# Performance work log

Measured on AMD Instinct MI355X. Metric: run time of the kernel, lower is better.

Reference implementation:

```python
import jax, jax.numpy as jnp
import numpy as np

N, E = 30000, 480000          # nodes, edges (avg degree 16)
DIM, DQK, H = 128, 128, 8     # dim_in = dim_v = 128, dim_qk = 128, heads
FD = DQK // H                 # kernel feature dim per head
DVH = DIM // H                # value dim per head


def setup_inputs() -> dict:
    key = jax.random.key(0)
    ks = jax.random.split(key, 12)
    g = lambda k, shape: jax.random.normal(k, shape, jnp.float32)
    return {
        "x": g(ks[0], (N, DIM)),
        "vec": g(ks[1], (N, 3, DIM)) * 0.1,
        "edge_vec": g(ks[2], (E, 3)),
        "edge_weight": jax.random.uniform(ks[3], (N, 1), jnp.float32),
        "W_fc1": g(ks[4], (DIM, 2 * DQK + DIM)) / np.sqrt(DIM),
        "W_fcv": g(ks[5], (DIM, 3 * DIM)) / np.sqrt(DIM),
        "b_fcv": jnp.zeros((3 * DIM,), jnp.float32),
        "W_fco": g(ks[6], (DIM, DIM)) / np.sqrt(DIM),
        "b_fco": jnp.zeros((DIM,), jnp.float32),
        "W_out": g(ks[7], (DIM, 3 * DIM)) / np.sqrt(DIM),
        "W_vecproj": g(ks[8], (DIM, 3 * DIM)) / np.sqrt(DIM),
        "W_equiv": g(ks[9], (DIM, DIM)) / np.sqrt(DIM),
        "ln_scale": jnp.ones((DIM,), jnp.float32),
        "ln_bias": jnp.zeros((DIM,), jnp.float32),
        "edge_index": jax.random.randint(ks[10], (2, E), 0, N),
    }


def _phi(z):
    # positive kernel feature map (elu + 1), per head: [N, DQK] -> [N, H, FD]
    return jax.nn.elu(z.reshape(z.shape[0], H, FD)) + 1.0


def reference(x, vec, edge_vec, edge_weight,
              W_fc1, W_fcv, b_fcv, W_fco, b_fco, W_out, W_vecproj, W_equiv,
              ln_scale, ln_bias, edge_index):
    # fc_1 -> q | k | non-attention residual
    h1 = x @ W_fc1
    q, k, non_att = h1[:, :DQK], h1[:, DQK:2 * DQK], h1[:, 2 * DQK:]
    # fc_v -> v | vec1 gate | vec2 gate
    pv = x @ W_fcv + b_fcv
    v, vec1, vec2 = pv[:, :DIM], pv[:, DIM:2 * DIM], pv[:, 2 * DIM:]

    # kernelized linear self-attention over the node set (order 1->1)
    qf, kf = _phi(q), _phi(k)                      # [N,H,FD]
    vh = v.reshape(N, H, DVH)                      # [N,H,DVH]
    kv = jnp.einsum('nhf,nhd->hfd', kf, vh)        # [H,FD,DVH]
    z = kf.sum(0)                                  # [H,FD]
    num = jnp.einsum('nhf,hfd->nhd', qf, kv)
    den = jnp.einsum('nhf,hf->nh', qf, z)[..., None] + 1e-6
    att = (num / den).reshape(N, DIM)

    # equivariant vector projections: v1p, v2p, v3p
    vp = jnp.einsum('nci,io->nco', vec, W_vecproj)  # [N,3,3*DIM]
    v1p, v2p, v3p = vp[..., :DIM], vp[..., DIM:2 * DIM], vp[..., 2 * DIM:]
    vec_dot = (v1p * v2p).sum(1)                    # [N,DIM]

    # MPNN propagate: per-edge vector messages, scatter-sum to destination
    src, dst = edge_index[0], edge_index[1]
    msg = vec[src] * vec1[src][:, None, :] + edge_vec[:, :, None] * vec2[src][:, None, :]
    vec_agg = jax.ops.segment_sum(msg, dst, num_segments=N)  # [N,3,DIM]

    # gated output combination (o1, o2, o3)
    o = att @ W_out
    o1, o2, o3 = o[:, :DIM], o[:, DIM:2 * DIM], o[:, 2 * DIM:]
    delta_x = vec_dot * o2 + o3
    delta_vec = v3p * o1[:, None, :] + vec_agg

    att_out = ((att + delta_x) @ W_fco + b_fco) * edge_weight
    out_x = non_att + att_out

    # LayerNorm over channel dim, then equivariant projection
    mu = delta_vec.mean(-1, keepdims=True)
    var = delta_vec.var(-1, keepdims=True)
    dvn = (delta_vec - mu) / jnp.sqrt(var + 1e-5) * ln_scale + ln_bias
    out_vec = dvn @ W_equiv
    return out_x, out_vec
```

## Files before the change

### kernel.cpp

```cpp
#include <hip/hip_runtime.h>
#include <math.h>

#define NN 30000
#define EE 480000
#define DIM 128
#define KVB 512

typedef __attribute__((ext_vector_type(8))) short bf16x8;
typedef __attribute__((ext_vector_type(4))) short s16x4;
typedef __attribute__((ext_vector_type(4))) float f32x4;
typedef __attribute__((ext_vector_type(4))) float float4v;

__device__ inline short f2bf(float f) {
    union { float f; unsigned u; } v; v.f = f;
    unsigned u = v.u;
    u += 0x7fffu + ((u >> 16) & 1u);
    return (short)(u >> 16);
}
__device__ inline float bf2f(unsigned short u) {
    union { unsigned u; float f; } v; v.u = ((unsigned)u) << 16; return v.f;
}

__device__ inline bf16x8 cvt8(float4v lo, float4v hi) {
    bf16x8 r;
    r[0] = f2bf(lo[0]); r[1] = f2bf(lo[1]); r[2] = f2bf(lo[2]); r[3] = f2bf(lo[3]);
    r[4] = f2bf(hi[0]); r[5] = f2bf(hi[1]); r[6] = f2bf(hi[2]); r[7] = f2bf(hi[3]);
    return r;
}

__global__ void pack_all(const float* __restrict__ fc1, const float* __restrict__ fcv,
                         const float* __restrict__ wout, const float* __restrict__ wvp,
                         const float* __restrict__ fco, const float* __restrict__ weq,
                         short* __restrict__ Wpk) {
    int fid = blockIdx.x * 4 + (threadIdx.x >> 6);
    int lane = threadIdx.x & 63;
    const float* src; int Nsrc, c0, f;
    if (fid < 96)       { src = fc1;  Nsrc = 384; c0 = 0;   f = fid; }
    else if (fid < 192) { src = fcv;  Nsrc = 384; c0 = 0;   f = fid - 96; }
    else if (fid < 288) { src = wout; Nsrc = 384; c0 = 0;   f = fid - 192; }
    else if (fid < 352) { src = wvp;  Nsrc = 384; c0 = 0;   f = fid - 288; }
    else if (fid < 384) { src = wvp;  Nsrc = 384; c0 = 256; f = fid - 352; }
    else if (fid < 416) { src = fco;  Nsrc = 128; c0 = 0;   f = fid - 384; }
    else                { src = weq;  Nsrc = 128; c0 = 0;   f = fid - 416; }
    int ct = f >> 2, kk = f & 3;
    int k0 = kk * 32 + (lane >> 4) * 8;
    int col = c0 + ct * 16 + (lane & 15);
    bf16x8 v;
#pragma unroll
    for (int i = 0; i < 8; ++i) v[i] = f2bf(src[(size_t)(k0 + i) * Nsrc + col]);
    *(bf16x8*)(Wpk + ((size_t)fid * 64 + lane) * 8) = v;
}

template<int COLS, int CT_PER, bool BIAS, typename InT, typename OutT>
__global__ __launch_bounds__(256) void mfma_gemm(const InT* __restrict__ in,
        const short* __restrict__ Wpk, const float* __restrict__ bias,
        OutT* __restrict__ out, int nrows) {
    const int lane = threadIdx.x & 63;
    const int wid = threadIdx.x >> 6;
    const int rbase = blockIdx.x * 128 + wid * 32;
    if (rbase >= nrows) return;
    const int ct0 = blockIdx.y * CT_PER;
    const int rlo = lane & 15, khi = (lane >> 4) * 8;
    bf16x8 a[2][4];
#pragma unroll
    for (int t = 0; t < 2; ++t) {
        int row = min(rbase + t * 16 + rlo, nrows - 1);
        const InT* rp = in + (size_t)row * 128 + khi;
#pragma unroll
        for (int kk = 0; kk < 4; ++kk) {
            if constexpr (sizeof(InT) == 4) {
                float4v lo = *(const float4v*)(rp + kk * 32);
                float4v hi = *(const float4v*)(rp + kk * 32 + 4);
                a[t][kk] = cvt8(lo, hi);
            } else {
                a[t][kk] = *(const bf16x8*)(rp + kk * 32);
            }
        }
    }
#pragma unroll
    for (int c = 0; c < CT_PER; ++c) {
        const int ct = ct0 + c;
        bf16x8 b[4];
#pragma unroll
        for (int kk = 0; kk < 4; ++kk)
            b[kk] = *(const bf16x8*)(Wpk + ((size_t)(ct * 4 + kk) * 64 + lane) * 8);
        f32x4 acc0 = {0.f, 0.f, 0.f, 0.f}, acc1 = {0.f, 0.f, 0.f, 0.f};
#pragma unroll
        for (int kk = 0; kk < 4; ++kk) {
            acc0 = __builtin_amdgcn_mfma_f32_16x16x32_bf16(a[0][kk], b[kk], acc0, 0, 0, 0);
            acc1 = __builtin_amdgcn_mfma_f32_16x16x32_bf16(a[1][kk], b[kk], acc1, 0, 0, 0);
        }
        const int col = ct * 16 + rlo;
        const float bv = BIAS ? bias[col] : 0.f;
#pragma unroll
        for (int r = 0; r < 4; ++r) {
            int row0 = rbase + (lane >> 4) * 4 + r;
            int row1 = row0 + 16;
            if constexpr (sizeof(OutT) == 4) {
                if (row0 < nrows) out[(size_t)row0 * COLS + col] = acc0[r] + bv;
                if (row1 < nrows) out[(size_t)row1 * COLS + col] = acc1[r] + bv;
            } else {
                if (row0 < nrows) out[(size_t)row0 * COLS + col] = (OutT)f2bf(acc0[r] + bv);
                if (row1 < nrows) out[(size_t)row1 * COLS + col] = (OutT)f2bf(acc1[r] + bv);
            }
        }
    }
}

__global__ __launch_bounds__(256) void kv_part(const float* __restrict__ h1,
        const float* __restrict__ pv, float* __restrict__ slab) {
    __shared__ float kf_s[8][DIM];
    __shared__ float v_s[8][DIM];
    const int tid = threadIdx.x;
    const int rpb = (NN + KVB - 1) / KVB;
    const int n0 = blockIdx.x * rpb;
    const int n1 = min(n0 + rpb, NN);
    const int base = tid * 8;
    const int hf = base >> 4;
    const int h = hf >> 4;
    const int d0 = base & 15;
    const int lr = tid >> 5;
    const int lg = tid & 31;
    const bool isK = lg < 16;
    const int le = (lg & 15) * 8;
    float acc[8];
#pragma unroll
    for (int i = 0; i < 8; ++i) acc[i] = 0.f;
    float zacc = 0.f;
    float4v p0 = {0,0,0,0}, p1 = {0,0,0,0};
    bool pvalid = false;
    {
        int n = n0 + lr;
        pvalid = n < n1;
        if (pvalid) {
            const float* src = isK ? (h1 + (size_t)n * 384 + 128 + le)
                                   : (pv + (size_t)n * 384 + le);
            p0 = *(const float4v*)src;
            p1 = *(const float4v*)(src + 4);
        }
    }
    for (int nt = n0; nt < n1; nt += 8) {
        __syncthreads();
        float4v c0 = p0, c1 = p1;
        if (!pvalid) { c0 = {0,0,0,0}; c1 = {0,0,0,0}; }
        else if (isK) {
#pragma unroll
            for (int i = 0; i < 4; ++i) {
                c0[i] = c0[i] > 0.f ? c0[i] + 1.f : expf(c0[i]);
                c1[i] = c1[i] > 0.f ? c1[i] + 1.f : expf(c1[i]);
            }
        }
        float* dst = (isK ? kf_s[lr] : v_s[lr]) + le;
        *(float4v*)dst = c0;
        *(float4v*)(dst + 4) = c1;
        __syncthreads();
        {
            int n = nt + 8 + lr;
            pvalid = n < n1;
            if (pvalid) {
                const float* src = isK ? (h1 + (size_t)n * 384 + 128 + le)
                                       : (pv + (size_t)n * 384 + le);
                p0 = *(const float4v*)src;
                p1 = *(const float4v*)(src + 4);
            }
        }
#pragma unroll
        for (int r = 0; r < 8; ++r) {
            float kfv = kf_s[r][hf];
#pragma unroll
            for (int i = 0; i < 8; ++i) acc[i] = fmaf(kfv, v_s[r][h * 16 + d0 + i], acc[i]);
            if (tid < 128) zacc += kf_s[r][tid];
        }
    }
    float* row = slab + (size_t)blockIdx.x * 2176;
#pragma unroll
    for (int i = 0; i < 8; ++i) row[base + i] = acc[i];
    if (tid < 128) row[2048 + tid] = zacc;
}

__global__ void kv_final(const float* __restrict__ slab, float* __restrict__ kvz) {
    int i = blockIdx.x * 256 + threadIdx.x;
    if (i >= 2176) return;
    float a[8];
#pragma unroll
    for (int j = 0; j < 8; ++j) a[j] = 0.f;
    for (int b = 0; b < KVB; b += 8) {
#pragma unroll
        for (int j = 0; j < 8; ++j) a[j] += slab[(size_t)(b + j) * 2176 + i];
    }
    kvz[i] = ((a[0] + a[1]) + (a[2] + a[3])) + ((a[4] + a[5]) + (a[6] + a[7]));
}

__global__ void attn_apply(const float* __restrict__ h1, const float* __restrict__ kvz,
                           unsigned short* __restrict__ att) {
    __shared__ float kv_s[8 * 16 * 17];
    __shared__ float z_s[DIM];
    __shared__ float qf_s[8][DIM];
    const int tid = threadIdx.x;
    const int n0 = blockIdx.x * 8;
    for (int i = tid; i < 2048; i += 128) {
        int hf = i >> 4, d = i & 15;
        kv_s[hf * 17 + d] = kvz[i];
    }
    z_s[tid] = kvz[2048 + tid];
#pragma unroll
    for (int r = 0; r < 8; ++r) {
        float qv = h1[(size_t)(n0 + r) * 384 + tid];
        qf_s[r][tid] = qv > 0.f ? qv + 1.f : expf(qv);
    }
    __syncthreads();
    const int h = tid >> 4, d = tid & 15;
#pragma unroll
    for (int r = 0; r < 8; ++r) {
        float num = 0.f, den = 0.f;
#pragma unroll
        for (int f = 0; f < 16; ++f) {
            float q = qf_s[r][h * 16 + f];
            num = fmaf(q, kv_s[(h * 16 + f) * 17 + d], num);
            den = fmaf(q, z_s[h * 16 + f], den);
        }
        att[(size_t)(n0 + r) * DIM + tid] = (unsigned short)f2bf(num / (den + 1e-6f));
    }
}

__global__ void vecdot_reduce(const unsigned short* __restrict__ vp12,
                              const float* __restrict__ vec, const float* __restrict__ pv,
                              float* __restrict__ vdot, unsigned short* __restrict__ P) {
    const int tid = threadIdx.x;
    const int n0 = blockIdx.x * 8;
#pragma unroll
    for (int r = 0; r < 8; ++r) {
        int n = n0 + r;
        const unsigned short* vp = vp12 + (size_t)(3 * n) * 256;
        float acc = bf2f(vp[tid]) * bf2f(vp[128 + tid])
                  + bf2f(vp[256 + tid]) * bf2f(vp[384 + tid])
                  + bf2f(vp[512 + tid]) * bf2f(vp[640 + tid]);
        vdot[(size_t)n * DIM + tid] = acc;
        float v1 = pv[(size_t)n * 384 + 128 + tid];
        float v2 = pv[(size_t)n * 384 + 256 + tid];
        s16x4 pk;
        pk[0] = f2bf(v2);
        pk[1] = f2bf(vec[((size_t)n * 3 + 0) * DIM + tid] * v1);
        pk[2] = f2bf(vec[((size_t)n * 3 + 1) * DIM + tid] * v1);
        pk[3] = f2bf(vec[((size_t)n * 3 + 2) * DIM + tid] * v1);
        *(s16x4*)(P + (size_t)n * 512 + tid * 4) = pk;
    }
}

__global__ void hist_kernel(const int* __restrict__ eidx, int* __restrict__ cnt) {
    int e = blockIdx.x * 256 + threadIdx.x;
    if (e < EE) atomicAdd(&cnt[eidx[EE + e]], 1);
}

__global__ void scan_kernel(const int* __restrict__ cnt, int* __restrict__ off,
                            int* __restrict__ pos) {
    __shared__ int wsum[16];
    const int tid = threadIdx.x;
    const int lane = tid & 63, wv = tid >> 6;
    const int PER = 30;
    const int base = tid * PER;
    int local[PER];
    int s = 0;
#pragma unroll
    for (int i = 0; i < PER; ++i) {
        int idx = base + i;
        int c = (idx < NN) ? cnt[idx] : 0;
        local[i] = s;
        s += c;
    }
    int incl = s;
#pragma unroll
    for (int d = 1; d < 64; d <<= 1) {
        int v = __shfl_up(incl, d, 64);
        if (lane >= d) incl += v;
    }
    if (lane == 63) wsum[wv] = incl;
    __syncthreads();
    if (wv == 0 && lane < 16) {
        int v = wsum[lane];
        int iv = v;
#pragma unroll
        for (int d = 1; d < 16; d <<= 1) {
            int u = __shfl_up(iv, d, 16);
            if (lane >= d) iv += u;
        }
        wsum[lane] = iv - v;
    }
    __syncthreads();
    const int carry = wsum[wv] + (incl - s);
#pragma unroll
    for (int i = 0; i < PER; ++i) {
        int idx = base + i;
        if (idx < NN) {
            int v = carry + local[i];
            off[idx] = v;
            pos[idx] = v;
        }
    }
    if (tid == 1023) off[NN] = wsum[15] + incl;
}

__global__ void scatter_kernel(const int* __restrict__ eidx, const float* __restrict__ evec,
                               int* __restrict__ pos, int4* __restrict__ sorted4) {
    int e = blockIdx.x * 256 + threadIdx.x;
    if (e >= EE) return;
    int dst = eidx[EE + e];
    int src = eidx[e];
    float e0 = evec[(size_t)e * 3 + 0];
    float e1 = evec[(size_t)e * 3 + 1];
    float e2 = evec[(size_t)e * 3 + 2];
    int p = atomicAdd(&pos[dst], 1);
    sorted4[p] = make_int4(src, __float_as_int(e0), __float_as_int(e1), __float_as_int(e2));
}

__global__ __launch_bounds__(256) void edge_agg_kernel(
        const int* __restrict__ off, const int4* __restrict__ sorted4,
        const unsigned short* __restrict__ P, float* __restrict__ agg) {
    __shared__ int srcs[128];
    __shared__ float evs[3][128];
    __shared__ float part[3][128];
    const int dst = blockIdx.x;
    const int tid = threadIdx.x;
    const int g = tid >> 7, o = tid & 127;
    const int j0 = off[dst], j1 = off[dst + 1];
    float a0 = 0.f, a1 = 0.f, a2 = 0.f;
    for (int jt = j0; jt < j1; jt += 128) {
        const int m = min(128, j1 - jt);
        if (tid < m) {
            int4 w = sorted4[jt + tid];
            srcs[tid] = w.x;
            evs[0][tid] = __int_as_float(w.y);
            evs[1][tid] = __int_as_float(w.z);
            evs[2][tid] = __int_as_float(w.w);
        }
        __syncthreads();
        int jj = g;
        for (; jj + 14 < m; jj += 16) {
            s16x4 pk[8];
#pragma unroll
            for (int u = 0; u < 8; ++u)
                pk[u] = *(const s16x4*)(P + (size_t)srcs[jj + 2 * u] * 512 + o * 4);
#pragma unroll
            for (int u = 0; u < 8; ++u) {
                float v2 = bf2f((unsigned short)pk[u][0]);
                a0 += fmaf(evs[0][jj + 2 * u], v2, bf2f((unsigned short)pk[u][1]));
                a1 += fmaf(evs[1][jj + 2 * u], v2, bf2f((unsigned short)pk[u][2]));
                a2 += fmaf(evs[2][jj + 2 * u], v2, bf2f((unsigned short)pk[u][3]));
            }
        }
        for (; jj < m; jj += 2) {
            s16x4 pk = *(const s16x4*)(P + (size_t)srcs[jj] * 512 + o * 4);
            float v2 = bf2f((unsigned short)pk[0]);
            a0 += fmaf(evs[0][jj], v2, bf2f((unsigned short)pk[1]));
            a1 += fmaf(evs[1][jj], v2, bf2f((unsigned short)pk[2]));
            a2 += fmaf(evs[2][jj], v2, bf2f((unsigned short)pk[3]));
        }
        __syncthreads();
    }
    if (g == 1) { part[0][o] = a0; part[1][o] = a1; part[2][o] = a2; }
    __syncthreads();
    if (g == 0) {
        a0 += part[0][o]; a1 += part[1][o]; a2 += part[2][o];
        agg[((size_t)dst * 3 + 0) * DIM + o] = a0;
        agg[((size_t)dst * 3 + 1) * DIM + o] = a1;
        agg[((size_t)dst * 3 + 2) * DIM + o] = a2;
    }
}

__global__ __launch_bounds__(256) void outx_mfma(const unsigned short* __restrict__ att,
        const float* __restrict__ vdot, const float* __restrict__ o,
        const short* __restrict__ Wpk, const float* __restrict__ bfco,
        const float* __restrict__ h1, const float* __restrict__ ew,
        float* __restrict__ outx) {
    const int lane = threadIdx.x & 63;
    const int wid = threadIdx.x >> 6;
    const int rbase = blockIdx.x * 128 + wid * 32;
    if (rbase >= NN) return;
    const int ct0 = blockIdx.y * 4;
    const int rlo = lane & 15, khi = (lane >> 4) * 8;
    bf16x8 a[2][4];
#pragma unroll
    for (int t = 0; t < 2; ++t) {
        int row = min(rbase + t * 16 + rlo, NN - 1);
        const unsigned short* pa = att + (size_t)row * 128 + khi;
        const float* pd = vdot + (size_t)row * 128 + khi;
        const float* po = o + (size_t)row * 384 + khi;
#pragma unroll
        for (int kk = 0; kk < 4; ++kk) {
            int kb = kk * 32;
            bf16x8 av = *(const bf16x8*)(pa + kb);
            float4v al, ah;
#pragma unroll
            for (int i = 0; i < 4; ++i) {
                al[i] = bf2f((unsigned short)av[i]);
                ah[i] = bf2f((unsigned short)av[4 + i]);
            }
            float4v dl = *(const float4v*)(pd + kb), dh = *(const float4v*)(pd + kb + 4);
            float4v o2l = *(const float4v*)(po + kb + 128), o2h = *(const float4v*)(po + kb + 132);
            float4v o3l = *(const float4v*)(po + kb + 256), o3h = *(const float4v*)(po + kb + 260);
            a[t][kk] = cvt8(al + dl * o2l + o3l, ah + dh * o2h + o3h);
        }
    }
    float ewv[2][4];
#pragma unroll
    for (int t = 0; t < 2; ++t)
#pragma unroll
        for (int r = 0; r < 4; ++r)
            ewv[t][r] = ew[min(rbase + t * 16 + (lane >> 4) * 4 + r, NN - 1)];
#pragma unroll
    for (int c = 0; c < 4; ++c) {
        const int ct = ct0 + c;
        bf16x8 b[4];
#pragma unroll
        for (int kk = 0; kk < 4; ++kk)
            b[kk] = *(const bf16x8*)(Wpk + ((size_t)(ct * 4 + kk) * 64 + lane) * 8);
        f32x4 acc0 = {0.f, 0.f, 0.f, 0.f}, acc1 = {0.f, 0.f, 0.f, 0.f};
#pragma unroll
        for (int kk = 0; kk < 4; ++kk) {
            acc0 = __builtin_amdgcn_mfma_f32_16x16x32_bf16(a[0][kk], b[kk], acc0, 0, 0, 0);
            acc1 = __builtin_amdgcn_mfma_f32_16x16x32_bf16(a[1][kk], b[kk], acc1, 0, 0, 0);
        }
        const int col = ct * 16 + rlo;
        const float bv = bfco[col];
#pragma unroll
        for (int r = 0; r < 4; ++r) {
            int row0 = rbase + (lane >> 4) * 4 + r;
            if (row0 < NN)
                outx[(size_t)row0 * 128 + col] =
                    h1[(size_t)row0 * 384 + 256 + col] + (acc0[r] + bv) * ewv[0][r];
            int row1 = row0 + 16;
            if (row1 < NN)
                outx[(size_t)row1 * 128 + col] =
                    h1[(size_t)row1 * 384 + 256 + col] + (acc1[r] + bv) * ewv[1][r];
        }
    }
}

__global__ __launch_bounds__(256) void outvec1(const float* __restrict__ vec,
        const short* __restrict__ Wpk3, const float* __restrict__ o,
        const float* __restrict__ agg, const float* __restrict__ ln_scale,
        const float* __restrict__ ln_bias, unsigned short* __restrict__ dvn) {
    const int NR = 3 * NN;
    const int lane = threadIdx.x & 63;
    const int wid = threadIdx.x >> 6;
    const int rbase = blockIdx.x * 128 + wid * 32;
    if (rbase >= NR) return;
    const int rlo = lane & 15, khi = (lane >> 4) * 8;
    bf16x8 a[2][4];
#pragma unroll
    for (int t = 0; t < 2; ++t) {
        int row = min(rbase + t * 16 + rlo, NR - 1);
        const float* rp = vec + (size_t)row * 128 + khi;
#pragma unroll
        for (int kk = 0; kk < 4; ++kk) {
            float4v lo = *(const float4v*)(rp + kk * 32);
            float4v hi = *(const float4v*)(rp + kk * 32 + 4);
            a[t][kk] = cvt8(lo, hi);
        }
    }
    f32x4 acc[2][8];
#pragma unroll
    for (int ct = 0; ct < 8; ++ct) {
        bf16x8 b[4];
#pragma unroll
        for (int kk = 0; kk < 4; ++kk)
            b[kk] = *(const bf16x8*)(Wpk3 + ((size_t)(ct * 4 + kk) * 64 + lane) * 8);
        f32x4 a0 = {0.f, 0.f, 0.f, 0.f}, a1 = {0.f, 0.f, 0.f, 0.f};
#pragma unroll
        for (int kk = 0; kk < 4; ++kk) {
            a0 = __builtin_amdgcn_mfma_f32_16x16x32_bf16(a[0][kk], b[kk], a0, 0, 0, 0);
            a1 = __builtin_amdgcn_mfma_f32_16x16x32_bf16(a[1][kk], b[kk], a1, 0, 0, 0);
        }
        acc[0][ct] = a0; acc[1][ct] = a1;
    }
    float s[2][4], s2[2][4];
#pragma unroll
    for (int t = 0; t < 2; ++t)
#pragma unroll
        for (int r = 0; r < 4; ++r) { s[t][r] = 0.f; s2[t][r] = 0.f; }
#pragma unroll
    for (int t = 0; t < 2; ++t)
#pragma unroll
        for (int r = 0; r < 4; ++r) {
            int row = min(rbase + t * 16 + (lane >> 4) * 4 + r, NR - 1);
            int n = row / 3;
#pragma unroll
            for (int ct = 0; ct < 8; ++ct) {
                int col = ct * 16 + rlo;
                float dv = acc[t][ct][r] * o[(size_t)n * 384 + col]
                         + agg[(size_t)row * 128 + col];
                acc[t][ct][r] = dv;
                s[t][r] += dv;
                s2[t][r] = fmaf(dv, dv, s2[t][r]);
            }
        }
#pragma unroll
    for (int t = 0; t < 2; ++t)
#pragma unroll
        for (int r = 0; r < 4; ++r) {
#pragma unroll
            for (int m = 1; m < 16; m <<= 1) {
                s[t][r] += __shfl_xor(s[t][r], m, 16);
                s2[t][r] += __shfl_xor(s2[t][r], m, 16);
            }
        }
#pragma unroll
    for (int t = 0; t < 2; ++t)
#pragma unroll
        for (int r = 0; r < 4; ++r) {
            int row = rbase + t * 16 + (lane >> 4) * 4 + r;
            if (row >= NR) continue;
            float mu = s[t][r] * (1.f / 128.f);
            float rstd = rsqrtf(s2[t][r] * (1.f / 128.f) - mu * mu + 1e-5f);
#pragma unroll
            for (int ct = 0; ct < 8; ++ct) {
                int col = ct * 16 + rlo;
                dvn[(size_t)row * 128 + col] =
                    (unsigned short)f2bf(fmaf((acc[t][ct][r] - mu) * rstd, ln_scale[col], ln_bias[col]));
            }
        }
}

extern "C" void kernel_launch(void* const* d_in, const int* in_sizes, int n_in,
                              void* d_out, int out_size, void* d_ws, size_t ws_size,
                              hipStream_t stream) {
    const float* x          = (const float*)d_in[0];
    const float* vec        = (const float*)d_in[1];
    const float* edge_vec   = (const float*)d_in[2];
    const float* edge_weight= (const float*)d_in[3];
    const float* W_fc1      = (const float*)d_in[4];
    const float* W_fcv      = (const float*)d_in[5];
    const float* b_fcv      = (const float*)d_in[6];
    const float* W_fco      = (const float*)d_in[7];
    const float* b_fco      = (const float*)d_in[8];
    const float* W_out      = (const float*)d_in[9];
    const float* W_vecproj  = (const float*)d_in[10];
    const float* W_equiv    = (const float*)d_in[11];
    const float* ln_scale   = (const float*)d_in[12];
    const float* ln_bias    = (const float*)d_in[13];
    const int*   edge_index = (const int*)d_in[14];

    float* out_x   = (float*)d_out;
    float* out_vec = out_x + (size_t)NN * DIM;
    unsigned short* Pb = (unsigned short*)d_out;

    float* ws   = (float*)d_ws;
    float* h1   = ws;
    float* pv   = h1 + 11520000;
    float* att  = pv + 11520000;
    float* vdot = att + 3840000;
    float* o    = vdot + 3840000;
    float* agg  = o + 11520000;
    float* kvz  = agg + 11520000;
    unsigned short* att_b = (unsigned short*)att;
    unsigned short* vp12b = (unsigned short*)o;
    unsigned short* dvnb  = (unsigned short*)pv;
    float* slab = agg;
    int* cnt    = (int*)(kvz + 2176);
    int* off    = cnt + NN;
    int* pos    = off + NN + 1;
    size_t soff = ((size_t)(pos + NN - (int*)ws) + 3) & ~(size_t)3;
    int4* sorted4 = (int4*)((int*)ws + soff);
    short* Wpk  = (short*)((int*)ws + soff + (size_t)4 * EE);
    short* pk_fc1  = Wpk;
    short* pk_fcv  = Wpk + 96 * 512;
    short* pk_wout = Wpk + 192 * 512;
    short* pk_vp12 = Wpk + 288 * 512;
    short* pk_vp3  = Wpk + 352 * 512;
    short* pk_fco  = Wpk + 384 * 512;
    short* pk_weq  = Wpk + 416 * 512;

    hipMemsetAsync(cnt, 0, NN * sizeof(int), stream);

    pack_all<<<112, 256, 0, stream>>>(W_fc1, W_fcv, W_out, W_vecproj, W_fco, W_equiv, Wpk);

    hist_kernel<<<(EE + 255) / 256, 256, 0, stream>>>(edge_index, cnt);
    scan_kernel<<<1, 1024, 0, stream>>>(cnt, off, pos);
    scatter_kernel<<<(EE + 255) / 256, 256, 0, stream>>>(edge_index, edge_vec, pos, sorted4);

    const int gN = (NN + 127) / 128;
    const int g3N = (3 * NN + 127) / 128;
    mfma_gemm<384, 8, false, float, float><<<dim3(gN, 3), 256, 0, stream>>>(x, pk_fc1, nullptr, h1, NN);
    mfma_gemm<384, 8, true, float, float><<<dim3(gN, 3), 256, 0, stream>>>(x, pk_fcv, b_fcv, pv, NN);
    kv_part<<<KVB, 256, 0, stream>>>(h1, pv, slab);
    kv_final<<<9, 256, 0, stream>>>(slab, kvz);
    attn_apply<<<NN / 8, 128, 0, stream>>>(h1, kvz, att_b);
    mfma_gemm<256, 8, false, float, unsigned short><<<dim3(g3N, 2), 256, 0, stream>>>(vec, pk_vp12, nullptr, vp12b, 3 * NN);
    vecdot_reduce<<<NN / 8, 128, 0, stream>>>(vp12b, vec, pv, vdot, Pb);
    mfma_gemm<384, 8, false, unsigned short, float><<<dim3(gN, 3), 256, 0, stream>>>(att_b, pk_wout, nullptr, o, NN);
    edge_agg_kernel<<<NN, 256, 0, stream>>>(off, sorted4, Pb, agg);
    outx_mfma<<<dim3(gN, 2), 256, 0, stream>>>(att_b, vdot, o, pk_fco, b_fco, h1, edge_weight, out_x);
    outvec1<<<g3N, 256, 0, stream>>>(vec, pk_vp3, o, agg, ln_scale, ln_bias, dvnb);
    mfma_gemm<128, 4, false, unsigned short, float><<<dim3(g3N, 2), 256, 0, stream>>>(dvnb, pk_weq, nullptr, out_vec, 3 * NN);
}
```

Baseline: 454.0 us.

## Compute v3p once in merged vecproj GEMM and store intermediates in bf16

Merges the v1p/v2p and v3p projections into one GEMM that writes bf16 vp12 and v3p, so outvec no longer recomputes the v3p GEMM. The LayerNorm stage becomes a lightweight elementwise kernel. The o, vdot and agg intermediates are stored as bf16 instead of fp32 to cut memory traffic. edge_agg is split across two blocks per destination with four edge groups, and vecdot_reduce uses vectorised loads. This adds bf16 rounding to more intermediates, which costs some precision.

```diff
diff --git a/kernel.cpp b/kernel.cpp
--- a/kernel.cpp
+++ b/kernel.cpp
@@ -7,9 +7,11 @@
 #define KVB 512
 
 typedef __attribute__((ext_vector_type(8))) short bf16x8;
+typedef __attribute__((ext_vector_type(8))) short s16x8;
 typedef __attribute__((ext_vector_type(4))) short s16x4;
 typedef __attribute__((ext_vector_type(4))) float f32x4;
 typedef __attribute__((ext_vector_type(4))) float float4v;
+typedef unsigned short ushort_t;
 
 __device__ inline short f2bf(float f) {
     union { float f; unsigned u; } v; v.f = f;
@@ -20,12 +22,22 @@
 __device__ inline float bf2f(unsigned short u) {
     union { unsigned u; float f; } v; v.u = ((unsigned)u) << 16; return v.f;
 }
+__device__ inline unsigned pack2(float a, float b) {
+    return (unsigned)(ushort_t)f2bf(a) | ((unsigned)(ushort_t)f2bf(b) << 16);
+}
 
 __device__ inline bf16x8 cvt8(float4v lo, float4v hi) {
     bf16x8 r;
     r[0] = f2bf(lo[0]); r[1] = f2bf(lo[1]); r[2] = f2bf(lo[2]); r[3] = f2bf(lo[3]);
     r[4] = f2bf(hi[0]); r[5] = f2bf(hi[1]); r[6] = f2bf(hi[2]); r[7] = f2bf(hi[3]);
     return r;
+}
+__device__ inline void bf8_to_f(bf16x8 v, float4v& lo, float4v& hi) {
+#pragma unroll
+    for (int i = 0; i < 4; ++i) {
+        lo[i] = bf2f((unsigned short)v[i]);
+        hi[i] = bf2f((unsigned short)v[4 + i]);
+    }
 }
 
 __global__ void pack_all(const float* __restrict__ fc1, const float* __restrict__ fcv,
@@ -107,6 +119,56 @@
     }
 }
 
+__global__ __launch_bounds__(256) void vp_gemm(const float* __restrict__ in,
+        const short* __restrict__ Wpk, ushort_t* __restrict__ vp12,
+        ushort_t* __restrict__ v3p, int nrows) {
+    const int lane = threadIdx.x & 63;
+    const int wid = threadIdx.x >> 6;
+    const int rbase = blockIdx.x * 128 + wid * 32;
+    if (rbase >= nrows) return;
+    const int ct0 = blockIdx.y * 8;
+    const int rlo = lane & 15, khi = (lane >> 4) * 8;
+    bf16x8 a[2][4];
+#pragma unroll
+    for (int t = 0; t < 2; ++t) {
+        int row = min(rbase + t * 16 + rlo, nrows - 1);
+        const float* rp = in + (size_t)row * 128 + khi;
+#pragma unroll
+        for (int kk = 0; kk < 4; ++kk) {
+            float4v lo = *(const float4v*)(rp + kk * 32);
+            float4v hi = *(const float4v*)(rp + kk * 32 + 4);
+            a[t][kk] = cvt8(lo, hi);
+        }
+    }
+#pragma unroll
+    for (int c = 0; c < 8; ++c) {
+        const int ct = ct0 + c;
+        bf16x8 b[4];
+#pragma unroll
+        for (int kk = 0; kk < 4; ++kk)
+            b[kk] = *(const bf16x8*)(Wpk + ((size_t)(ct * 4 + kk) * 64 + lane) * 8);
+        f32x4 acc0 = {0.f, 0.f, 0.f, 0.f}, acc1 = {0.f, 0.f, 0.f, 0.f};
+#pragma unroll
+        for (int kk = 0; kk < 4; ++kk) {
+            acc0 = __builtin_amdgcn_mfma_f32_16x16x32_bf16(a[0][kk], b[kk], acc0, 0, 0, 0);
+            acc1 = __builtin_amdgcn_mfma_f32_16x16x32_bf16(a[1][kk], b[kk], acc1, 0, 0, 0);
+        }
+        const int col = ct * 16 + rlo;
+#pragma unroll
+        for (int r = 0; r < 4; ++r) {
+            int row0 = rbase + (lane >> 4) * 4 + r;
+            int row1 = row0 + 16;
+            if (col < 256) {
+                if (row0 < nrows) vp12[(size_t)row0 * 256 + col] = (ushort_t)f2bf(acc0[r]);
+                if (row1 < nrows) vp12[(size_t)row1 * 256 + col] = (ushort_t)f2bf(acc1[r]);
+            } else {
+                if (row0 < nrows) v3p[(size_t)row0 * 128 + col - 256] = (ushort_t)f2bf(acc0[r]);
+                if (row1 < nrows) v3p[(size_t)row1 * 128 + col - 256] = (ushort_t)f2bf(acc1[r]);
+            }
+        }
+    }
+}
+
 __global__ __launch_bounds__(256) void kv_part(const float* __restrict__ h1,
         const float* __restrict__ pv, float* __restrict__ slab) {
     __shared__ float kf_s[8][DIM];
@@ -192,7 +254,7 @@
 }
 
 __global__ void attn_apply(const float* __restrict__ h1, const float* __restrict__ kvz,
-                           unsigned short* __restrict__ att) {
+                           ushort_t* __restrict__ att) {
     __shared__ float kv_s[8 * 16 * 17];
     __shared__ float z_s[DIM];
     __shared__ float qf_s[8][DIM];
@@ -219,31 +281,41 @@
             num = fmaf(q, kv_s[(h * 16 + f) * 17 + d], num);
             den = fmaf(q, z_s[h * 16 + f], den);
         }
-        att[(size_t)(n0 + r) * DIM + tid] = (unsigned short)f2bf(num / (den + 1e-6f));
-    }
-}
-
-__global__ void vecdot_reduce(const unsigned short* __restrict__ vp12,
-                              const float* __restrict__ vec, const float* __restrict__ pv,
-                              float* __restrict__ vdot, unsigned short* __restrict__ P) {
+        att[(size_t)(n0 + r) * DIM + tid] = (ushort_t)f2bf(num / (den + 1e-6f));
+    }
+}
+
+__global__ __launch_bounds__(256) void vecdot_reduce(const ushort_t* __restrict__ vp12,
+        const float* __restrict__ vec, const float* __restrict__ pv,
+        ushort_t* __restrict__ vdot, ushort_t* __restrict__ P) {
     const int tid = threadIdx.x;
+    const int c2 = tid & 63;
+    const int sub = tid >> 6;
     const int n0 = blockIdx.x * 8;
 #pragma unroll
-    for (int r = 0; r < 8; ++r) {
-        int n = n0 + r;
-        const unsigned short* vp = vp12 + (size_t)(3 * n) * 256;
-        float acc = bf2f(vp[tid]) * bf2f(vp[128 + tid])
-                  + bf2f(vp[256 + tid]) * bf2f(vp[384 + tid])
-                  + bf2f(vp[512 + tid]) * bf2f(vp[640 + tid]);
-        vdot[(size_t)n * DIM + tid] = acc;
-        float v1 = pv[(size_t)n * 384 + 128 + tid];
-        float v2 = pv[(size_t)n * 384 + 256 + tid];
-        s16x4 pk;
-        pk[0] = f2bf(v2);
-        pk[1] = f2bf(vec[((size_t)n * 3 + 0) * DIM + tid] * v1);
-        pk[2] = f2bf(vec[((size_t)n * 3 + 1) * DIM + tid] * v1);
-        pk[3] = f2bf(vec[((size_t)n * 3 + 2) * DIM + tid] * v1);
-        *(s16x4*)(P + (size_t)n * 512 + tid * 4) = pk;
+    for (int rr = 0; rr < 2; ++rr) {
+        const int n = n0 + sub + rr * 4;
+        float a0 = 0.f, a1 = 0.f;
+#pragma unroll
+        for (int c = 0; c < 3; ++c) {
+            unsigned u1 = *(const unsigned*)(vp12 + (size_t)(3 * n + c) * 256 + 2 * c2);
+            unsigned u2 = *(const unsigned*)(vp12 + (size_t)(3 * n + c) * 256 + 128 + 2 * c2);
+            a0 = fmaf(bf2f((unsigned short)u1), bf2f((unsigned short)u2), a0);
+            a1 = fmaf(bf2f((unsigned short)(u1 >> 16)), bf2f((unsigned short)(u2 >> 16)), a1);
+        }
+        *(unsigned*)(vdot + (size_t)n * 128 + 2 * c2) = pack2(a0, a1);
+        float2 v1 = *(const float2*)(pv + (size_t)n * 384 + 128 + 2 * c2);
+        float2 v2 = *(const float2*)(pv + (size_t)n * 384 + 256 + 2 * c2);
+        s16x8 pk;
+        pk[0] = f2bf(v2.x);
+        pk[4] = f2bf(v2.y);
+#pragma unroll
+        for (int c = 0; c < 3; ++c) {
+            float2 vc = *(const float2*)(vec + ((size_t)n * 3 + c) * 128 + 2 * c2);
+            pk[1 + c] = f2bf(vc.x * v1.x);
+            pk[5 + c] = f2bf(vc.y * v1.y);
+        }
+        *(s16x8*)(P + (size_t)n * 512 + (size_t)c2 * 8) = pk;
     }
 }
 
@@ -315,13 +387,14 @@
 
 __global__ __launch_bounds__(256) void edge_agg_kernel(
         const int* __restrict__ off, const int4* __restrict__ sorted4,
-        const unsigned short* __restrict__ P, float* __restrict__ agg) {
+        const ushort_t* __restrict__ P, ushort_t* __restrict__ agg) {
     __shared__ int srcs[128];
     __shared__ float evs[3][128];
-    __shared__ float part[3][128];
+    __shared__ float part[3][3][64];
     const int dst = blockIdx.x;
     const int tid = threadIdx.x;
-    const int g = tid >> 7, o = tid & 127;
+    const int g = tid >> 6, l = tid & 63;
+    const int o = blockIdx.y * 64 + l;
     const int j0 = off[dst], j1 = off[dst + 1];
     float a0 = 0.f, a1 = 0.f, a2 = 0.f;
     for (int jt = j0; jt < j1; jt += 128) {
@@ -335,20 +408,21 @@
         }
         __syncthreads();
         int jj = g;
-        for (; jj + 14 < m; jj += 16) {
+        for (; jj + 28 < m; jj += 32) {
             s16x4 pk[8];
 #pragma unroll
             for (int u = 0; u < 8; ++u)
-                pk[u] = *(const s16x4*)(P + (size_t)srcs[jj + 2 * u] * 512 + o * 4);
+                pk[u] = *(const s16x4*)(P + (size_t)srcs[jj + 4 * u] * 512 + o * 4);
 #pragma unroll
             for (int u = 0; u < 8; ++u) {
+                int e = jj + 4 * u;
                 float v2 = bf2f((unsigned short)pk[u][0]);
-                a0 += fmaf(evs[0][jj + 2 * u], v2, bf2f((unsigned short)pk[u][1]));
-                a1 += fmaf(evs[1][jj + 2 * u], v2, bf2f((unsigned short)pk[u][2]));
-                a2 += fmaf(evs[2][jj + 2 * u], v2, bf2f((unsigned short)pk[u][3]));
+                a0 += fmaf(evs[0][e], v2, bf2f((unsigned short)pk[u][1]));
+                a1 += fmaf(evs[1][e], v2, bf2f((unsigned short)pk[u][2]));
+                a2 += fmaf(evs[2][e], v2, bf2f((unsigned short)pk[u][3]));
             }
         }
-        for (; jj < m; jj += 2) {
+        for (; jj < m; jj += 4) {
             s16x4 pk = *(const s16x4*)(P + (size_t)srcs[jj] * 512 + o * 4);
             float v2 = bf2f((unsigned short)pk[0]);
             a0 += fmaf(evs[0][jj], v2, bf2f((unsigned short)pk[1]));
@@ -357,18 +431,20 @@
         }
         __syncthreads();
     }
-    if (g == 1) { part[0][o] = a0; part[1][o] = a1; part[2][o] = a2; }
+    if (g) { part[g - 1][0][l] = a0; part[g - 1][1][l] = a1; part[g - 1][2][l] = a2; }
     __syncthreads();
     if (g == 0) {
-        a0 += part[0][o]; a1 += part[1][o]; a2 += part[2][o];
-        agg[((size_t)dst * 3 + 0) * DIM + o] = a0;
-        agg[((size_t)dst * 3 + 1) * DIM + o] = a1;
-        agg[((size_t)dst * 3 + 2) * DIM + o] = a2;
-    }
-}
-
-__global__ __launch_bounds__(256) void outx_mfma(const unsigned short* __restrict__ att,
-        const float* __restrict__ vdot, const float* __restrict__ o,
+        a0 += part[0][0][l] + part[1][0][l] + part[2][0][l];
+        a1 += part[0][1][l] + part[1][1][l] + part[2][1][l];
+        a2 += part[0][2][l] + part[1][2][l] + part[2][2][l];
+        agg[((size_t)dst * 3 + 0) * DIM + o] = (ushort_t)f2bf(a0);
+        agg[((size_t)dst * 3 + 1) * DIM + o] = (ushort_t)f2bf(a1);
+        agg[((size_t)dst * 3 + 2) * DIM + o] = (ushort_t)f2bf(a2);
+    }
+}
+
+__global__ __launch_bounds__(256) void outx_mfma(const ushort_t* __restrict__ att,
+        const ushort_t* __restrict__ vdot, const ushort_t* __restrict__ o,
         const short* __restrict__ Wpk, const float* __restrict__ bfco,
         const float* __restrict__ h1, const float* __restrict__ ew,
         float* __restrict__ outx) {
@@ -382,22 +458,17 @@
 #pragma unroll
     for (int t = 0; t < 2; ++t) {
         int row = min(rbase + t * 16 + rlo, NN - 1);
-        const unsigned short* pa = att + (size_t)row * 128 + khi;
-        const float* pd = vdot + (size_t)row * 128 + khi;
-        const float* po = o + (size_t)row * 384 + khi;
+        const ushort_t* pa = att + (size_t)row * 128 + khi;
+        const ushort_t* pd = vdot + (size_t)row * 128 + khi;
+        const ushort_t* po = o + (size_t)row * 384 + khi;
 #pragma unroll
         for (int kk = 0; kk < 4; ++kk) {
             int kb = kk * 32;
-            bf16x8 av = *(const bf16x8*)(pa + kb);
-            float4v al, ah;
-#pragma unroll
-            for (int i = 0; i < 4; ++i) {
-                al[i] = bf2f((unsigned short)av[i]);
-                ah[i] = bf2f((unsigned short)av[4 + i]);
-            }
-            float4v dl = *(const float4v*)(pd + kb), dh = *(const float4v*)(pd + kb + 4);
-            float4v o2l = *(const float4v*)(po + kb + 128), o2h = *(const float4v*)(po + kb + 132);
-            float4v o3l = *(const float4v*)(po + kb + 256), o3h = *(const float4v*)(po + kb + 260);
+            float4v al, ah, dl, dh, o2l, o2h, o3l, o3h;
+            bf8_to_f(*(const bf16x8*)(pa + kb), al, ah);
+            bf8_to_f(*(const bf16x8*)(pd + kb), dl, dh);
+            bf8_to_f(*(const bf16x8*)(po + 128 + kb), o2l, o2h);
+            bf8_to_f(*(const bf16x8*)(po + 256 + kb), o3l, o3h);
             a[t][kk] = cvt8(al + dl * o2l + o3l, ah + dh * o2h + o3h);
         }
     }
@@ -436,89 +507,33 @@
     }
 }
 
-__global__ __launch_bounds__(256) void outvec1(const float* __restrict__ vec,
-        const short* __restrict__ Wpk3, const float* __restrict__ o,
-        const float* __restrict__ agg, const float* __restrict__ ln_scale,
-        const float* __restrict__ ln_bias, unsigned short* __restrict__ dvn) {
-    const int NR = 3 * NN;
-    const int lane = threadIdx.x & 63;
-    const int wid = threadIdx.x >> 6;
-    const int rbase = blockIdx.x * 128 + wid * 32;
-    if (rbase >= NR) return;
-    const int rlo = lane & 15, khi = (lane >> 4) * 8;
-    bf16x8 a[2][4];
-#pragma unroll
-    for (int t = 0; t < 2; ++t) {
-        int row = min(rbase + t * 16 + rlo, NR - 1);
-        const float* rp = vec + (size_t)row * 128 + khi;
-#pragma unroll
-        for (int kk = 0; kk < 4; ++kk) {
-            float4v lo = *(const float4v*)(rp + kk * 32);
-            float4v hi = *(const float4v*)(rp + kk * 32 + 4);
-            a[t][kk] = cvt8(lo, hi);
-        }
-    }
-    f32x4 acc[2][8];
-#pragma unroll
-    for (int ct = 0; ct < 8; ++ct) {
-        bf16x8 b[4];
-#pragma unroll
-        for (int kk = 0; kk < 4; ++kk)
-            b[kk] = *(const bf16x8*)(Wpk3 + ((size_t)(ct * 4 + kk) * 64 + lane) * 8);
-        f32x4 a0 = {0.f, 0.f, 0.f, 0.f}, a1 = {0.f, 0.f, 0.f, 0.f};
-#pragma unroll
-        for (int kk = 0; kk < 4; ++kk) {
-            a0 = __builtin_amdgcn_mfma_f32_16x16x32_bf16(a[0][kk], b[kk], a0, 0, 0, 0);
-            a1 = __builtin_amdgcn_mfma_f32_16x16x32_bf16(a[1][kk], b[kk], a1, 0, 0, 0);
-        }
-        acc[0][ct] = a0; acc[1][ct] = a1;
-    }
-    float s[2][4], s2[2][4];
-#pragma unroll
-    for (int t = 0; t < 2; ++t)
-#pragma unroll
-        for (int r = 0; r < 4; ++r) { s[t][r] = 0.f; s2[t][r] = 0.f; }
-#pragma unroll
-    for (int t = 0; t < 2; ++t)
-#pragma unroll
-        for (int r = 0; r < 4; ++r) {
-            int row = min(rbase + t * 16 + (lane >> 4) * 4 + r, NR - 1);
-            int n = row / 3;
-#pragma unroll
-            for (int ct = 0; ct < 8; ++ct) {
-                int col = ct * 16 + rlo;
-                float dv = acc[t][ct][r] * o[(size_t)n * 384 + col]
-                         + agg[(size_t)row * 128 + col];
-                acc[t][ct][r] = dv;
-                s[t][r] += dv;
-                s2[t][r] = fmaf(dv, dv, s2[t][r]);
-            }
-        }
-#pragma unroll
-    for (int t = 0; t < 2; ++t)
-#pragma unroll
-        for (int r = 0; r < 4; ++r) {
-#pragma unroll
-            for (int m = 1; m < 16; m <<= 1) {
-                s[t][r] += __shfl_xor(s[t][r], m, 16);
-                s2[t][r] += __shfl_xor(s2[t][r], m, 16);
-            }
-        }
-#pragma unroll
-    for (int t = 0; t < 2; ++t)
-#pragma unroll
-        for (int r = 0; r < 4; ++r) {
-            int row = rbase + t * 16 + (lane >> 4) * 4 + r;
-            if (row >= NR) continue;
-            float mu = s[t][r] * (1.f / 128.f);
-            float rstd = rsqrtf(s2[t][r] * (1.f / 128.f) - mu * mu + 1e-5f);
-#pragma unroll
-            for (int ct = 0; ct < 8; ++ct) {
-                int col = ct * 16 + rlo;
-                dvn[(size_t)row * 128 + col] =
-                    (unsigned short)f2bf(fmaf((acc[t][ct][r] - mu) * rstd, ln_scale[col], ln_bias[col]));
-            }
-        }
+__global__ __launch_bounds__(256) void outvec_ln(const ushort_t* __restrict__ v3p,
+        const ushort_t* __restrict__ o, const ushort_t* __restrict__ agg,
+        const float* __restrict__ ln_scale, const float* __restrict__ ln_bias,
+        ushort_t* __restrict__ dvn) {
+    const int tid = threadIdx.x;
+    const int c2 = tid & 63;
+    const int row = blockIdx.x * 4 + (tid >> 6);
+    const int n = row / 3;
+    unsigned uv3 = *(const unsigned*)(v3p + (size_t)row * 128 + 2 * c2);
+    unsigned uo1 = *(const unsigned*)(o + (size_t)n * 384 + 2 * c2);
+    unsigned uag = *(const unsigned*)(agg + (size_t)row * 128 + 2 * c2);
+    float dv0 = fmaf(bf2f((unsigned short)uv3), bf2f((unsigned short)uo1),
+                     bf2f((unsigned short)uag));
+    float dv1 = fmaf(bf2f((unsigned short)(uv3 >> 16)), bf2f((unsigned short)(uo1 >> 16)),
+                     bf2f((unsigned short)(uag >> 16)));
+    float s = dv0 + dv1;
+    float s2 = fmaf(dv0, dv0, dv1 * dv1);
+#pragma unroll
+    for (int d = 1; d < 64; d <<= 1) {
+        s += __shfl_xor(s, d, 64);
+        s2 += __shfl_xor(s2, d, 64);
+    }
+    float mu = s * (1.f / 128.f);
+    float rstd = rsqrtf(s2 * (1.f / 128.f) - mu * mu + 1e-5f);
+    float r0 = fmaf((dv0 - mu) * rstd, ln_scale[2 * c2], ln_bias[2 * c2]);
+    float r1 = fmaf((dv1 - mu) * rstd, ln_scale[2 * c2 + 1], ln_bias[2 * c2 + 1]);
+    *(unsigned*)(dvn + (size_t)row * 128 + 2 * c2) = pack2(r0, r1);
 }
 
 extern "C" void kernel_launch(void* const* d_in, const int* in_sizes, int n_in,
@@ -542,20 +557,20 @@
 
     float* out_x   = (float*)d_out;
     float* out_vec = out_x + (size_t)NN * DIM;
-    unsigned short* Pb = (unsigned short*)d_out;
+    ushort_t* Pb = (ushort_t*)d_out;
 
     float* ws   = (float*)d_ws;
     float* h1   = ws;
     float* pv   = h1 + 11520000;
-    float* att  = pv + 11520000;
-    float* vdot = att + 3840000;
-    float* o    = vdot + 3840000;
-    float* agg  = o + 11520000;
-    float* kvz  = agg + 11520000;
-    unsigned short* att_b = (unsigned short*)att;
-    unsigned short* vp12b = (unsigned short*)o;
-    unsigned short* dvnb  = (unsigned short*)pv;
-    float* slab = agg;
+    ushort_t* att_b  = (ushort_t*)(pv + 11520000);
+    ushort_t* vdot_b = att_b + 3840000;
+    ushort_t* o_b    = vdot_b + 3840000;
+    ushort_t* agg_b  = o_b + 11520000;
+    ushort_t* v3p_b  = agg_b + 11520000;
+    float* kvz  = (float*)(v3p_b + 11520000);
+    ushort_t* vp12_b = o_b;
+    float* slab = (float*)o_b;
+    ushort_t* dvn_b = (ushort_t*)pv;
     int* cnt    = (int*)(kvz + 2176);
     int* off    = cnt + NN;
     int* pos    = off + NN + 1;
@@ -565,8 +580,7 @@
     short* pk_fc1  = Wpk;
     short* pk_fcv  = Wpk + 96 * 512;
     short* pk_wout = Wpk + 192 * 512;
-    short* pk_vp12 = Wpk + 288 * 512;
-    short* pk_vp3  = Wpk + 352 * 512;
+    short* pk_vp   = Wpk + 288 * 512;
     short* pk_fco  = Wpk + 384 * 512;
     short* pk_weq  = Wpk + 416 * 512;
 
@@ -585,11 +599,11 @@
     kv_part<<<KVB, 256, 0, stream>>>(h1, pv, slab);
     kv_final<<<9, 256, 0, stream>>>(slab, kvz);
     attn_apply<<<NN / 8, 128, 0, stream>>>(h1, kvz, att_b);
-    mfma_gemm<256, 8, false, float, unsigned short><<<dim3(g3N, 2), 256, 0, stream>>>(vec, pk_vp12, nullptr, vp12b, 3 * NN);
-    vecdot_reduce<<<NN / 8, 128, 0, stream>>>(vp12b, vec, pv, vdot, Pb);
-    mfma_gemm<384, 8, false, unsigned short, float><<<dim3(gN, 3), 256, 0, stream>>>(att_b, pk_wout, nullptr, o, NN);
-    edge_agg_kernel<<<NN, 256, 0, stream>>>(off, sorted4, Pb, agg);
-    outx_mfma<<<dim3(gN, 2), 256, 0, stream>>>(att_b, vdot, o, pk_fco, b_fco, h1, edge_weight, out_x);
-    outvec1<<<g3N, 256, 0, stream>>>(vec, pk_vp3, o, agg, ln_scale, ln_bias, dvnb);
-    mfma_gemm<128, 4, false, unsigned short, float><<<dim3(g3N, 2), 256, 0, stream>>>(dvnb, pk_weq, nullptr, out_vec, 3 * NN);
-}
+    vp_gemm<<<dim3(g3N, 3), 256, 0, stream>>>(vec, pk_vp, vp12_b, v3p_b, 3 * NN);
+    vecdot_reduce<<<NN / 8, 256, 0, stream>>>(vp12_b, vec, pv, vdot_b, Pb);
+    mfma_gemm<384, 8, false, ushort_t, ushort_t><<<dim3(gN, 3), 256, 0, stream>>>(att_b, pk_wout, nullptr, o_b, NN);
+    edge_agg_kernel<<<dim3(NN, 2), 256, 0, stream>>>(off, sorted4, Pb, agg_b);
+    outx_mfma<<<dim3(gN, 2), 256, 0, stream>>>(att_b, vdot_b, o_b, pk_fco, b_fco, h1, edge_weight, out_x);
+    outvec_ln<<<(3 * NN) / 4, 256, 0, stream>>>(v3p_b, o_b, agg_b, ln_scale, ln_bias, dvn_b);
+    mfma_gemm<128, 4, false, ushort_t, float><<<dim3(g3N, 2), 256, 0, stream>>>(dvn_b, pk_weq, nullptr, out_vec, 3 * NN);
+}
```

Result: slower. 468.8 us (+3.2%).
